# Performance work log

Hardware: AMD Instinct MI355X
Metric: run time of the kernel (lower is better)

## Reference

```python
import jax, jax.numpy as jnp
import numpy as np

N = 50000
E = 800000
D = 128  # input_dim = hidden_dim = output_dim
N_LAYERS = 3


def _graph_conv(x, src, dst, edge_weight, w_rel, b_rel, w_root):
    # PyG GraphConv (aggr='add'):
    #   out = lin_rel( sum_{j in N(i)} edge_weight_ij * x_j ) + lin_root(x_i)
    msg = x[src] * edge_weight[:, None]                      # [E, D_in]
    agg = jax.ops.segment_sum(msg, dst, num_segments=x.shape[0])  # [N, D_in]
    return agg @ w_rel + b_rel + x @ w_root                  # [N, D_out]


def setup_inputs() -> dict:
    key = jax.random.key(0)
    ks = jax.random.split(key, 4 + 3 * N_LAYERS)
    x = jax.random.normal(ks[0], (N, D), dtype=jnp.float32)
    edge_index = jax.random.randint(ks[1], (2, E), 0, N, dtype=jnp.int32)
    edge_attr = jax.random.uniform(ks[2], (E,), dtype=jnp.float32)
    scale = 1.0 / np.sqrt(D)
    inp = {"x": x, "edge_index": edge_index, "edge_attr": edge_attr}
    for l in range(N_LAYERS):
        inp[f"w_rel{l}"] = jax.random.normal(ks[3 + 3 * l], (D, D), dtype=jnp.float32) * scale
        inp[f"b_rel{l}"] = jnp.zeros((D,), dtype=jnp.float32)
        inp[f"w_root{l}"] = jax.random.normal(ks[4 + 3 * l], (D, D), dtype=jnp.float32) * scale
    return inp


def reference(x, edge_index, edge_attr,
              w_rel0, b_rel0, w_root0,
              w_rel1, b_rel1, w_root1,
              w_rel2, b_rel2, w_root2):
    src, dst = edge_index[0], edge_index[1]
    params = [(w_rel0, b_rel0, w_root0), (w_rel1, b_rel1, w_root1), (w_rel2, b_rel2, w_root2)]
    h = x
    for w_rel, b_rel, w_root in params[:-1]:
        h = _graph_conv(h, src, dst, edge_attr, w_rel, b_rel, w_root)
        h = jax.nn.relu(h)  # dropout p=0.0 -> identity
    w_rel, b_rel, w_root = params[-1]
    return _graph_conv(h, src, dst, edge_attr, w_rel, b_rel, w_root)
```

## Files before the change

### kernel.cpp

```cpp
#include <hip/hip_runtime.h>
#include <hip/hip_bf16.h>
#include <hip/hip_fp16.h>

#define N_NODES 50000
#define N_EDGES 800000
#define DIM 128

#define NBUCK 391
#define BCAP  2816
#define CHUNK 2048

#define CVT_BLOCKS 25000

#define LDSROW 136

typedef float floatx4 __attribute__((ext_vector_type(4)));
typedef float floatx2 __attribute__((ext_vector_type(2)));
typedef short shortx8 __attribute__((ext_vector_type(8)));

__device__ __forceinline__ unsigned short f2bf(float f) {
    union { float f; unsigned int u; } c; c.f = f;
    unsigned int u = c.u;
    unsigned int r = (u + 0x7FFFu + ((u >> 16) & 1u)) >> 16;
    return (unsigned short)r;
}
__device__ __forceinline__ floatx2 bf2x2(unsigned int p) {
    union { unsigned int u; float f; } lo, hi;
    lo.u = p << 16; hi.u = p & 0xFFFF0000u;
    return (floatx2){lo.f, hi.f};
}

__global__ __launch_bounds__(256)
void prep_kernel(const float* __restrict__ x, unsigned short* __restrict__ X,
                 const float* __restrict__ wr0, const float* __restrict__ wt0,
                 const float* __restrict__ wr1, const float* __restrict__ wt1,
                 const float* __restrict__ wr2, const float* __restrict__ wt2,
                 unsigned short* __restrict__ Wp, int* __restrict__ bcursor) {
    int b = blockIdx.x;
    if (b < CVT_BLOCKS) {
        int i = b * 256 + threadIdx.x;
        X[i] = f2bf(x[i]);
    } else if (b == CVT_BLOCKS) {
        for (int i = threadIdx.x; i < NBUCK; i += 256) bcursor[i] = 0;
    } else {
        int id = (b - CVT_BLOCKS - 1) * 256 + threadIdx.x;
        int layer = id >> 15;
        int rem = id & 32767;
        int j  = rem & 7;
        int L  = (rem >> 3) & 63;
        int ct = (rem >> 9) & 7;
        int t  = rem >> 12;
        int k = t * 32 + (L >> 4) * 8 + j;
        int c = ct * 16 + (L & 15);
        const float* wr = (layer == 0) ? wr0 : (layer == 1) ? wr1 : wr2;
        const float* wt = (layer == 0) ? wt0 : (layer == 1) ? wt1 : wt2;
        float v = (k < 128) ? wr[k * 128 + c] : wt[(k - 128) * 128 + c];
        Wp[id] = f2bf(v);
    }
}

__global__ __launch_bounds__(512)
void partition_kernel(const int* __restrict__ src, const int* __restrict__ dst,
                      const float* __restrict__ ew,
                      int* __restrict__ bcursor, int2* __restrict__ bstage, int e) {
    __shared__ int2 stage[CHUNK];
    __shared__ int cnt[NBUCK];
    __shared__ int lbase[NBUCK];
    __shared__ int gbase[NBUCK];
    __shared__ int wsum[8];
    const int tid = threadIdx.x;
    const int e0 = blockIdx.x * CHUNK;
    const int ecnt = min(CHUNK, e - e0);

    for (int i = tid; i < NBUCK; i += 512) cnt[i] = 0;
    __syncthreads();
    for (int i = tid; i < ecnt; i += 512)
        atomicAdd(&cnt[dst[e0 + i] >> 7], 1);
    __syncthreads();

    {
        int v = (tid < NBUCK) ? cnt[tid] : 0;
        int lane = tid & 63, wid = tid >> 6;
        int acc = v;
#pragma unroll
        for (int off = 1; off < 64; off <<= 1) {
            int t = __shfl_up(acc, off, 64);
            if (lane >= off) acc += t;
        }
        if (lane == 63) wsum[wid] = acc;
        __syncthreads();
        int wpref = 0;
        for (int w = 0; w < wid; ++w) wpref += wsum[w];
        int excl = wpref + acc - v;
        if (tid < NBUCK) {
            lbase[tid] = excl;
            gbase[tid] = atomicAdd(&bcursor[tid], v);
            cnt[tid] = 0;
        }
    }
    __syncthreads();

    for (int i = tid; i < ecnt; i += 512) {
        int d = dst[e0 + i];
        int s = src[e0 + i];
        unsigned int hw = (unsigned int)__half_as_ushort(__float2half(ew[e0 + i]));
        int b = d >> 7;
        int pos = atomicAdd(&cnt[b], 1);
        stage[lbase[b] + pos] = make_int2((int)((hw << 16) | (unsigned int)s), d);
    }
    __syncthreads();

    for (int j = tid; j < ecnt; j += 512) {
        int2 p = stage[j];
        int b = p.y >> 7;
        int gidx = b * BCAP + gbase[b] + (j - lbase[b]);
        bstage[gidx] = p;
    }
}

__global__ __launch_bounds__(256)
void bucket_fill_kernel(const int2* __restrict__ bstage, const int* __restrict__ bcursor,
                        int* __restrict__ row_start, unsigned int* __restrict__ perm4, int n) {
    __shared__ int cnt128[128];
    __shared__ int curs[128];
    __shared__ int wsum[4];
    __shared__ int sbase, scnt;
    const int tid = threadIdx.x;
    const int b = blockIdx.x;
    const int node0 = b << 7;
    const int lane = tid & 63, wid = tid >> 6;

    {
        int i0 = tid * 2, i1 = tid * 2 + 1;
        int v0 = (i0 < NBUCK) ? bcursor[i0] : 0;
        int v1 = (i1 < NBUCK) ? bcursor[i1] : 0;
        int s = v0 + v1;
        int acc = s;
#pragma unroll
        for (int off = 1; off < 64; off <<= 1) {
            int t = __shfl_up(acc, off, 64);
            if (lane >= off) acc += t;
        }
        if (lane == 63) wsum[wid] = acc;
        __syncthreads();
        int wpref = 0;
        for (int w = 0; w < wid; ++w) wpref += wsum[w];
        int excl = wpref + acc - s;
        if (i0 == b) { sbase = excl;      scnt = v0; }
        if (i1 == b) { sbase = excl + v0; scnt = v1; }
    }
    __syncthreads();
    const int cntb = scnt;
    const int base = sbase;
    const int2* sp = bstage + (size_t)b * BCAP;

    if (tid < 128) cnt128[tid] = 0;
    __syncthreads();
    for (int i = tid; i < cntb; i += 256)
        atomicAdd(&cnt128[sp[i].y & 127], 1);
    __syncthreads();

    int v = (tid < 128) ? cnt128[tid] : 0;
    int acc = v;
#pragma unroll
    for (int off = 1; off < 64; off <<= 1) {
        int t = __shfl_up(acc, off, 64);
        if (lane >= off) acc += t;
    }
    if (lane == 63) wsum[wid] = acc;
    __syncthreads();
    int wpref = 0;
    for (int w = 0; w < wid; ++w) wpref += wsum[w];
    int excl = wpref + acc - v;
    if (tid < 128) {
        int node = node0 + tid;
        if (node <= n) row_start[node] = base + excl;
        curs[tid] = excl;
    }
    __syncthreads();

    for (int i = tid; i < cntb; i += 256) {
        int2 p = sp[i];
        int pos = atomicAdd(&curs[p.y & 127], 1);
        perm4[base + pos] = (unsigned int)p.x;
    }
}

__global__ __launch_bounds__(256, 8)
void fused_layer(const unsigned short* __restrict__ h, const int* __restrict__ row_start,
                 const unsigned int* __restrict__ perm4, const unsigned short* __restrict__ Wp,
                 const float* __restrict__ bias, float* __restrict__ outF,
                 unsigned short* __restrict__ outB, int n, int relu) {
    __shared__ unsigned short Gs[16 * LDSROW];
    const int tid  = threadIdx.x;
    const int lane = tid & 63;
    const int wid  = tid >> 6;
    const int g  = lane >> 4;
    const int sl = lane & 15;
    const int rowT = blockIdx.x * 16;
    const int nodeBase = rowT + wid * 4;

    int rs = 0;
    if (lane < 5) {
        int idx = nodeBase + lane;
        rs = row_start[idx <= n ? idx : n];
    }

    for (int nd = 0; nd < 4; ++nd) {
        if (nodeBase + nd >= n) break;
        int beg = __shfl(rs, nd, 64);
        int end = __shfl(rs, nd + 1, 64);
        floatx2 ac[4];
#pragma unroll
        for (int k = 0; k < 4; ++k) ac[k] = (floatx2){0.f, 0.f};
        for (int t = beg; t < end; t += 16) {
            int i0 = t + g, i1 = t + 4 + g, i2 = t + 8 + g, i3 = t + 12 + g;
            unsigned int p0 = (i0 < end) ? perm4[i0] : 0;
            unsigned int p1 = (i1 < end) ? perm4[i1] : 0;
            unsigned int p2 = (i2 < end) ? perm4[i2] : 0;
            unsigned int p3 = (i3 < end) ? perm4[i3] : 0;
            int s0 = p0 & 0xFFFF, s1 = p1 & 0xFFFF, s2 = p2 & 0xFFFF, s3 = p3 & 0xFFFF;
            uint4 v0 = *(const uint4*)(h + (size_t)s0 * DIM + sl * 8);
            uint4 v1 = *(const uint4*)(h + (size_t)s1 * DIM + sl * 8);
            uint4 v2 = *(const uint4*)(h + (size_t)s2 * DIM + sl * 8);
            uint4 v3 = *(const uint4*)(h + (size_t)s3 * DIM + sl * 8);
            float w0 = __half2float(__ushort_as_half((unsigned short)(p0 >> 16)));
            float w1 = __half2float(__ushort_as_half((unsigned short)(p1 >> 16)));
            float w2 = __half2float(__ushort_as_half((unsigned short)(p2 >> 16)));
            float w3 = __half2float(__ushort_as_half((unsigned short)(p3 >> 16)));
            floatx2 W0 = (floatx2){w0, w0}, W1 = (floatx2){w1, w1};
            floatx2 W2 = (floatx2){w2, w2}, W3 = (floatx2){w3, w3};
            ac[0] += W0 * bf2x2(v0.x); ac[1] += W0 * bf2x2(v0.y);
            ac[2] += W0 * bf2x2(v0.z); ac[3] += W0 * bf2x2(v0.w);
            ac[0] += W1 * bf2x2(v1.x); ac[1] += W1 * bf2x2(v1.y);
            ac[2] += W1 * bf2x2(v1.z); ac[3] += W1 * bf2x2(v1.w);
            ac[0] += W2 * bf2x2(v2.x); ac[1] += W2 * bf2x2(v2.y);
            ac[2] += W2 * bf2x2(v2.z); ac[3] += W2 * bf2x2(v2.w);
            ac[0] += W3 * bf2x2(v3.x); ac[1] += W3 * bf2x2(v3.y);
            ac[2] += W3 * bf2x2(v3.z); ac[3] += W3 * bf2x2(v3.w);
        }
        float acc[8] = {ac[0].x, ac[0].y, ac[1].x, ac[1].y,
                        ac[2].x, ac[2].y, ac[3].x, ac[3].y};
#pragma unroll
        for (int k = 0; k < 8; ++k) {
            acc[k] += __shfl_xor(acc[k], 16, 64);
            acc[k] += __shfl_xor(acc[k], 32, 64);
        }
        if (lane < 16) {
            uint4 r;
            r.x = (unsigned int)f2bf(acc[0]) | ((unsigned int)f2bf(acc[1]) << 16);
            r.y = (unsigned int)f2bf(acc[2]) | ((unsigned int)f2bf(acc[3]) << 16);
            r.z = (unsigned int)f2bf(acc[4]) | ((unsigned int)f2bf(acc[5]) << 16);
            r.w = (unsigned int)f2bf(acc[6]) | ((unsigned int)f2bf(acc[7]) << 16);
            *(uint4*)(&Gs[(wid * 4 + nd) * LDSROW + sl * 8]) = r;
        }
    }
    __syncthreads();

    floatx4 acc2[2];
#pragma unroll
    for (int ct = 0; ct < 2; ++ct) acc2[ct] = (floatx4){0.f, 0.f, 0.f, 0.f};

    int rGlob = rowT + sl;
    int rr = (rGlob < n) ? rGlob : (n - 1);
    const int ko = g * 8;
#pragma unroll
    for (int t = 0; t < 8; ++t) {
        shortx8 a;
        if (t < 4)
            a = *(const shortx8*)(&Gs[sl * LDSROW + t * 32 + ko]);
        else
            a = *(const shortx8*)(h + (size_t)rr * DIM + (t - 4) * 32 + ko);
        const unsigned short* wp = Wp + (size_t)t * 4096 + (wid * 2) * 512 + lane * 8;
#pragma unroll
        for (int ct = 0; ct < 2; ++ct) {
            shortx8 b = *(const shortx8*)(wp + ct * 512);
            acc2[ct] = __builtin_amdgcn_mfma_f32_16x16x32_bf16(a, b, acc2[ct], 0, 0, 0);
        }
    }

#pragma unroll
    for (int ct = 0; ct < 2; ++ct) {
        int col = wid * 32 + ct * 16 + sl;
        float bv = bias[col];
#pragma unroll
        for (int i = 0; i < 4; ++i) {
            int row = rowT + g * 4 + i;
            if (row < n) {
                float v = acc2[ct][i] + bv;
                if (relu) v = fmaxf(v, 0.f);
                if (outF) outF[(size_t)row * DIM + col] = v;
                else      outB[(size_t)row * DIM + col] = f2bf(v);
            }
        }
    }
}

extern "C" void kernel_launch(void* const* d_in, const int* in_sizes, int n_in,
                              void* d_out, int out_size, void* d_ws, size_t ws_size,
                              hipStream_t stream) {
    const int N = N_NODES, E = N_EDGES;

    const float* x   = (const float*)d_in[0];
    const int*   ei  = (const int*)d_in[1];
    const float* ea  = (const float*)d_in[2];
    const float* wr0 = (const float*)d_in[3];
    const float* br0 = (const float*)d_in[4];
    const float* wt0 = (const float*)d_in[5];
    const float* wr1 = (const float*)d_in[6];
    const float* br1 = (const float*)d_in[7];
    const float* wt1 = (const float*)d_in[8];
    const float* wr2 = (const float*)d_in[9];
    const float* br2 = (const float*)d_in[10];
    const float* wt2 = (const float*)d_in[11];
    const int* srcI = ei;
    const int* dstI = ei + E;
    float* out = (float*)d_out;

    int2* bstage = (int2*)d_ws;
    unsigned short* X  = (unsigned short*)(bstage + (size_t)NBUCK * BCAP);
    unsigned short* H1 = X + (size_t)N * DIM;
    unsigned short* H2 = H1 + (size_t)N * DIM;
    unsigned short* Wp = H2 + (size_t)N * DIM;
    unsigned int* perm4 = (unsigned int*)(Wp + 3 * 32768);
    int* bcursor = (int*)(perm4 + E);
    int* rowst   = bcursor + NBUCK;

    prep_kernel<<<CVT_BLOCKS + 1 + 384, 256, 0, stream>>>(x, X, wr0, wt0, wr1, wt1, wr2, wt2, Wp, bcursor);
    partition_kernel<<<(E + CHUNK - 1) / CHUNK, 512, 0, stream>>>(srcI, dstI, ea, bcursor, bstage, E);
    bucket_fill_kernel<<<NBUCK, 256, 0, stream>>>(bstage, bcursor, rowst, perm4, N);

    const int fusedGrid = (N + 15) / 16;

    fused_layer<<<fusedGrid, 256, 0, stream>>>(X,  rowst, perm4, Wp,         br0, nullptr, H1, N, 1);
    fused_layer<<<fusedGrid, 256, 0, stream>>>(H1, rowst, perm4, Wp + 32768, br1, nullptr, H2, N, 1);
    fused_layer<<<fusedGrid, 256, 0, stream>>>(H2, rowst, perm4, Wp + 65536, br2, out, nullptr, N, 0);
}
```

Before: 244.0 us.

## Assign one node per 16-lane group in gather, drop bounds checks, widen prep blocks

The aggregation loop in the fused layer now gives each 16-lane quarter-wave its own node. Before, all 64 lanes worked on one node at a time and then reduced across groups with cross-lane shuffles. This removes the shuffle reduction and the serial loop over four nodes, but a wave's runtime now follows the highest-degree node among its four. The N bounds checks are dropped because N is a multiple of 16, which hardcodes that assumption. The partition and bucket-fill kernels also double their block sizes, and bucket-fill's two-elements-per-thread prefix scan becomes one element per thread.

New measurement: 236.1 us. -3.3%, faster.

```diff
diff --git a/kernel.cpp b/kernel.cpp
--- a/kernel.cpp
+++ b/kernel.cpp
@@ -59,7 +59,7 @@
     }
 }
 
-__global__ __launch_bounds__(512)
+__global__ __launch_bounds__(1024)
 void partition_kernel(const int* __restrict__ src, const int* __restrict__ dst,
                       const float* __restrict__ ew,
                       int* __restrict__ bcursor, int2* __restrict__ bstage, int e) {
@@ -67,14 +67,14 @@
     __shared__ int cnt[NBUCK];
     __shared__ int lbase[NBUCK];
     __shared__ int gbase[NBUCK];
-    __shared__ int wsum[8];
+    __shared__ int wsum[16];
     const int tid = threadIdx.x;
     const int e0 = blockIdx.x * CHUNK;
     const int ecnt = min(CHUNK, e - e0);
 
-    for (int i = tid; i < NBUCK; i += 512) cnt[i] = 0;
-    __syncthreads();
-    for (int i = tid; i < ecnt; i += 512)
+    for (int i = tid; i < NBUCK; i += 1024) cnt[i] = 0;
+    __syncthreads();
+    for (int i = tid; i < ecnt; i += 1024)
         atomicAdd(&cnt[dst[e0 + i] >> 7], 1);
     __syncthreads();
 
@@ -100,7 +100,7 @@
     }
     __syncthreads();
 
-    for (int i = tid; i < ecnt; i += 512) {
+    for (int i = tid; i < ecnt; i += 1024) {
         int d = dst[e0 + i];
         int s = src[e0 + i];
         unsigned int hw = (unsigned int)__half_as_ushort(__float2half(ew[e0 + i]));
@@ -110,7 +110,7 @@
     }
     __syncthreads();
 
-    for (int j = tid; j < ecnt; j += 512) {
+    for (int j = tid; j < ecnt; j += 1024) {
         int2 p = stage[j];
         int b = p.y >> 7;
         int gidx = b * BCAP + gbase[b] + (j - lbase[b]);
@@ -118,12 +118,12 @@
     }
 }
 
-__global__ __launch_bounds__(256)
+__global__ __launch_bounds__(512)
 void bucket_fill_kernel(const int2* __restrict__ bstage, const int* __restrict__ bcursor,
                         int* __restrict__ row_start, unsigned int* __restrict__ perm4, int n) {
     __shared__ int cnt128[128];
     __shared__ int curs[128];
-    __shared__ int wsum[4];
+    __shared__ int wsum[8];
     __shared__ int sbase, scnt;
     const int tid = threadIdx.x;
     const int b = blockIdx.x;
@@ -131,11 +131,8 @@
     const int lane = tid & 63, wid = tid >> 6;
 
     {
-        int i0 = tid * 2, i1 = tid * 2 + 1;
-        int v0 = (i0 < NBUCK) ? bcursor[i0] : 0;
-        int v1 = (i1 < NBUCK) ? bcursor[i1] : 0;
-        int s = v0 + v1;
-        int acc = s;
+        int v = (tid < NBUCK) ? bcursor[tid] : 0;
+        int acc = v;
 #pragma unroll
         for (int off = 1; off < 64; off <<= 1) {
             int t = __shfl_up(acc, off, 64);
@@ -145,9 +142,8 @@
         __syncthreads();
         int wpref = 0;
         for (int w = 0; w < wid; ++w) wpref += wsum[w];
-        int excl = wpref + acc - s;
-        if (i0 == b) { sbase = excl;      scnt = v0; }
-        if (i1 == b) { sbase = excl + v0; scnt = v1; }
+        int excl = wpref + acc - v;
+        if (tid == b) { sbase = excl; scnt = v; }
     }
     __syncthreads();
     const int cntb = scnt;
@@ -156,7 +152,7 @@
 
     if (tid < 128) cnt128[tid] = 0;
     __syncthreads();
-    for (int i = tid; i < cntb; i += 256)
+    for (int i = tid; i < cntb; i += 512)
         atomicAdd(&cnt128[sp[i].y & 127], 1);
     __syncthreads();
 
@@ -179,7 +175,7 @@
     }
     __syncthreads();
 
-    for (int i = tid; i < cntb; i += 256) {
+    for (int i = tid; i < cntb; i += 512) {
         int2 p = sp[i];
         int pos = atomicAdd(&curs[p.y & 127], 1);
         perm4[base + pos] = (unsigned int)p.x;
@@ -190,7 +186,7 @@
 void fused_layer(const unsigned short* __restrict__ h, const int* __restrict__ row_start,
                  const unsigned int* __restrict__ perm4, const unsigned short* __restrict__ Wp,
                  const float* __restrict__ bias, float* __restrict__ outF,
-                 unsigned short* __restrict__ outB, int n, int relu) {
+                 unsigned short* __restrict__ outB, int relu) {
     __shared__ unsigned short Gs[16 * LDSROW];
     const int tid  = threadIdx.x;
     const int lane = tid & 63;
@@ -201,59 +197,45 @@
     const int nodeBase = rowT + wid * 4;
 
     int rs = 0;
-    if (lane < 5) {
-        int idx = nodeBase + lane;
-        rs = row_start[idx <= n ? idx : n];
-    }
-
-    for (int nd = 0; nd < 4; ++nd) {
-        if (nodeBase + nd >= n) break;
-        int beg = __shfl(rs, nd, 64);
-        int end = __shfl(rs, nd + 1, 64);
-        floatx2 ac[4];
-#pragma unroll
-        for (int k = 0; k < 4; ++k) ac[k] = (floatx2){0.f, 0.f};
-        for (int t = beg; t < end; t += 16) {
-            int i0 = t + g, i1 = t + 4 + g, i2 = t + 8 + g, i3 = t + 12 + g;
-            unsigned int p0 = (i0 < end) ? perm4[i0] : 0;
-            unsigned int p1 = (i1 < end) ? perm4[i1] : 0;
-            unsigned int p2 = (i2 < end) ? perm4[i2] : 0;
-            unsigned int p3 = (i3 < end) ? perm4[i3] : 0;
-            int s0 = p0 & 0xFFFF, s1 = p1 & 0xFFFF, s2 = p2 & 0xFFFF, s3 = p3 & 0xFFFF;
-            uint4 v0 = *(const uint4*)(h + (size_t)s0 * DIM + sl * 8);
-            uint4 v1 = *(const uint4*)(h + (size_t)s1 * DIM + sl * 8);
-            uint4 v2 = *(const uint4*)(h + (size_t)s2 * DIM + sl * 8);
-            uint4 v3 = *(const uint4*)(h + (size_t)s3 * DIM + sl * 8);
-            float w0 = __half2float(__ushort_as_half((unsigned short)(p0 >> 16)));
-            float w1 = __half2float(__ushort_as_half((unsigned short)(p1 >> 16)));
-            float w2 = __half2float(__ushort_as_half((unsigned short)(p2 >> 16)));
-            float w3 = __half2float(__ushort_as_half((unsigned short)(p3 >> 16)));
-            floatx2 W0 = (floatx2){w0, w0}, W1 = (floatx2){w1, w1};
-            floatx2 W2 = (floatx2){w2, w2}, W3 = (floatx2){w3, w3};
-            ac[0] += W0 * bf2x2(v0.x); ac[1] += W0 * bf2x2(v0.y);
-            ac[2] += W0 * bf2x2(v0.z); ac[3] += W0 * bf2x2(v0.w);
-            ac[0] += W1 * bf2x2(v1.x); ac[1] += W1 * bf2x2(v1.y);
-            ac[2] += W1 * bf2x2(v1.z); ac[3] += W1 * bf2x2(v1.w);
-            ac[0] += W2 * bf2x2(v2.x); ac[1] += W2 * bf2x2(v2.y);
-            ac[2] += W2 * bf2x2(v2.z); ac[3] += W2 * bf2x2(v2.w);
-            ac[0] += W3 * bf2x2(v3.x); ac[1] += W3 * bf2x2(v3.y);
-            ac[2] += W3 * bf2x2(v3.z); ac[3] += W3 * bf2x2(v3.w);
-        }
-        float acc[8] = {ac[0].x, ac[0].y, ac[1].x, ac[1].y,
-                        ac[2].x, ac[2].y, ac[3].x, ac[3].y};
-#pragma unroll
-        for (int k = 0; k < 8; ++k) {
-            acc[k] += __shfl_xor(acc[k], 16, 64);
-            acc[k] += __shfl_xor(acc[k], 32, 64);
-        }
-        if (lane < 16) {
-            uint4 r;
-            r.x = (unsigned int)f2bf(acc[0]) | ((unsigned int)f2bf(acc[1]) << 16);
-            r.y = (unsigned int)f2bf(acc[2]) | ((unsigned int)f2bf(acc[3]) << 16);
-            r.z = (unsigned int)f2bf(acc[4]) | ((unsigned int)f2bf(acc[5]) << 16);
-            r.w = (unsigned int)f2bf(acc[6]) | ((unsigned int)f2bf(acc[7]) << 16);
-            *(uint4*)(&Gs[(wid * 4 + nd) * LDSROW + sl * 8]) = r;
-        }
+    if (lane < 5) rs = row_start[nodeBase + lane];
+    const int beg = __shfl(rs, g, 64);
+    const int end = __shfl(rs, g + 1, 64);
+
+    floatx2 ac[4];
+#pragma unroll
+    for (int k = 0; k < 4; ++k) ac[k] = (floatx2){0.f, 0.f};
+    const unsigned short* hp = h + sl * 8;
+    for (int t = beg; t < end; t += 4) {
+        unsigned int p0 = perm4[t];
+        unsigned int p1 = (t + 1 < end) ? perm4[t + 1] : 0;
+        unsigned int p2 = (t + 2 < end) ? perm4[t + 2] : 0;
+        unsigned int p3 = (t + 3 < end) ? perm4[t + 3] : 0;
+        uint4 v0 = *(const uint4*)(hp + (size_t)(p0 & 0xFFFF) * DIM);
+        uint4 v1 = *(const uint4*)(hp + (size_t)(p1 & 0xFFFF) * DIM);
+        uint4 v2 = *(const uint4*)(hp + (size_t)(p2 & 0xFFFF) * DIM);
+        uint4 v3 = *(const uint4*)(hp + (size_t)(p3 & 0xFFFF) * DIM);
+        float w0 = __half2float(__ushort_as_half((unsigned short)(p0 >> 16)));
+        float w1 = __half2float(__ushort_as_half((unsigned short)(p1 >> 16)));
+        float w2 = __half2float(__ushort_as_half((unsigned short)(p2 >> 16)));
+        float w3 = __half2float(__ushort_as_half((unsigned short)(p3 >> 16)));
+        floatx2 W0 = (floatx2){w0, w0}, W1 = (floatx2){w1, w1};
+        floatx2 W2 = (floatx2){w2, w2}, W3 = (floatx2){w3, w3};
+        ac[0] += W0 * bf2x2(v0.x); ac[1] += W0 * bf2x2(v0.y);
+        ac[2] += W0 * bf2x2(v0.z); ac[3] += W0 * bf2x2(v0.w);
+        ac[0] += W1 * bf2x2(v1.x); ac[1] += W1 * bf2x2(v1.y);
+        ac[2] += W1 * bf2x2(v1.z); ac[3] += W1 * bf2x2(v1.w);
+        ac[0] += W2 * bf2x2(v2.x); ac[1] += W2 * bf2x2(v2.y);
+        ac[2] += W2 * bf2x2(v2.z); ac[3] += W2 * bf2x2(v2.w);
+        ac[0] += W3 * bf2x2(v3.x); ac[1] += W3 * bf2x2(v3.y);
+        ac[2] += W3 * bf2x2(v3.z); ac[3] += W3 * bf2x2(v3.w);
+    }
+    {
+        uint4 r;
+        r.x = (unsigned int)f2bf(ac[0].x) | ((unsigned int)f2bf(ac[0].y) << 16);
+        r.y = (unsigned int)f2bf(ac[1].x) | ((unsigned int)f2bf(ac[1].y) << 16);
+        r.z = (unsigned int)f2bf(ac[2].x) | ((unsigned int)f2bf(ac[2].y) << 16);
+        r.w = (unsigned int)f2bf(ac[3].x) | ((unsigned int)f2bf(ac[3].y) << 16);
+        *(uint4*)(&Gs[(wid * 4 + g) * LDSROW + sl * 8]) = r;
     }
     __syncthreads();
 
@@ -261,8 +243,7 @@
 #pragma unroll
     for (int ct = 0; ct < 2; ++ct) acc2[ct] = (floatx4){0.f, 0.f, 0.f, 0.f};
 
-    int rGlob = rowT + sl;
-    int rr = (rGlob < n) ? rGlob : (n - 1);
+    const int rr = rowT + sl;
     const int ko = g * 8;
 #pragma unroll
     for (int t = 0; t < 8; ++t) {
@@ -286,12 +267,10 @@
 #pragma unroll
         for (int i = 0; i < 4; ++i) {
             int row = rowT + g * 4 + i;
-            if (row < n) {
-                float v = acc2[ct][i] + bv;
-                if (relu) v = fmaxf(v, 0.f);
-                if (outF) outF[(size_t)row * DIM + col] = v;
-                else      outB[(size_t)row * DIM + col] = f2bf(v);
-            }
+            float v = acc2[ct][i] + bv;
+            if (relu) v = fmaxf(v, 0.f);
+            if (outF) outF[(size_t)row * DIM + col] = v;
+            else      outB[(size_t)row * DIM + col] = f2bf(v);
         }
     }
 }
@@ -327,12 +306,12 @@
     int* rowst   = bcursor + NBUCK;
 
     prep_kernel<<<CVT_BLOCKS + 1 + 384, 256, 0, stream>>>(x, X, wr0, wt0, wr1, wt1, wr2, wt2, Wp, bcursor);
-    partition_kernel<<<(E + CHUNK - 1) / CHUNK, 512, 0, stream>>>(srcI, dstI, ea, bcursor, bstage, E);
-    bucket_fill_kernel<<<NBUCK, 256, 0, stream>>>(bstage, bcursor, rowst, perm4, N);
-
-    const int fusedGrid = (N + 15) / 16;
-
-    fused_layer<<<fusedGrid, 256, 0, stream>>>(X,  rowst, perm4, Wp,         br0, nullptr, H1, N, 1);
-    fused_layer<<<fusedGrid, 256, 0, stream>>>(H1, rowst, perm4, Wp + 32768, br1, nullptr, H2, N, 1);
-    fused_layer<<<fusedGrid, 256, 0, stream>>>(H2, rowst, perm4, Wp + 65536, br2, out, nullptr, N, 0);
-}
+    partition_kernel<<<(E + CHUNK - 1) / CHUNK, 1024, 0, stream>>>(srcI, dstI, ea, bcursor, bstage, E);
+    bucket_fill_kernel<<<NBUCK, 512, 0, stream>>>(bstage, bcursor, rowst, perm4, N);
+
+    const int fusedGrid = N / 16;
+
+    fused_layer<<<fusedGrid, 256, 0, stream>>>(X,  rowst, perm4, Wp,         br0, nullptr, H1, 1);
+    fused_layer<<<fusedGrid, 256, 0, stream>>>(H1, rowst, perm4, Wp + 32768, br1, nullptr, H2, 1);
+    fused_layer<<<fusedGrid, 256, 0, stream>>>(H2, rowst, perm4, Wp + 65536, br2, out, nullptr, 0);
+}
```
